# Performance work log

Measured on AMD Instinct MI355X. Metric: run time of the kernel, lower is better.

The kernel has to match this reference:

```python
import jax, jax.numpy as jnp
import numpy as np

# Problem geometry: B graphs of M atoms each (batch = repeat(arange(B), M)).
B, M, K = 1024, 256, 32          # graphs, atoms/graph, max_num_neighbors
CUTOFF_LOWER = 0.0
CUTOFF_UPPER = 5.0
BOX = 16.0                        # box side so ~30 neighbors within cutoff
BIG = 1e9                         # sentinel distance^2 for masked pairs


def setup_inputs() -> dict:
    key = jax.random.key(0)
    pos = jax.random.uniform(key, (B * M, 3), dtype=jnp.float32) * BOX
    batch = jnp.repeat(jnp.arange(B, dtype=jnp.int32), M)
    return {"pos": pos, "batch": batch}


def reference(pos, batch):
    # Fixed-size, jit-compatible radius_graph: per node keep the K nearest
    # neighbors within CUTOFF_UPPER (no self loops, loop=False). Invalid
    # (padded) edges get index -1, weight 0, vec 0.
    p = pos.reshape(B, M, 3)
    sq = jnp.sum(p * p, axis=-1)                                  # [B,M]
    d2 = sq[:, :, None] + sq[:, None, :] - 2.0 * jnp.einsum(
        'bmd,bnd->bmn', p, p)                                     # [B,M,M]
    d2 = jnp.maximum(d2, 0.0)
    self_mask = jnp.eye(M, dtype=bool)[None]
    invalid = self_mask | (d2 >= CUTOFF_UPPER ** 2)
    d2m = jnp.where(invalid, BIG, d2)
    neg_d2_sel, idx = jax.lax.top_k(-d2m, K)                      # [B,M,K]
    d2_sel = -neg_d2_sel
    valid = d2_sel < CUTOFF_UPPER ** 2
    w = jnp.sqrt(jnp.where(valid, d2_sel, 1.0))                   # safe sqrt
    valid = valid & (w >= CUTOFF_LOWER)                           # lower cutoff
    w = jnp.where(valid, w, 0.0)
    # edge_vec = pos[edge0] - pos[edge1] with edge0 = neighbor, edge1 = center
    nbr = jax.vmap(lambda pb, ib: pb[ib])(p, idx)                 # [B,M,K,3]
    vec = jnp.where(valid[..., None], nbr - p[:, :, None, :], 0.0)
    offs = (jnp.arange(B, dtype=jnp.int32) * M)[:, None, None]
    nbr_g = jnp.where(valid, idx.astype(jnp.int32) + offs, -1)
    ctr_g = jnp.where(
        valid, jnp.arange(M, dtype=jnp.int32)[None, :, None] + offs, -1)
    edge_index = jnp.stack([nbr_g.reshape(-1), ctr_g.reshape(-1)])  # [2, B*M*K]
    edge_weight = w.reshape(-1)                                     # [B*M*K]
    edge_vec = vec.reshape(-1, 3)                                   # [B*M*K,3]
    return edge_index, edge_weight, edge_vec
```

## Files before the change

### kernel.cpp

```cpp
#include <hip/hip_runtime.h>
#include <hip/hip_bf16.h>
#include <stdint.h>

#define NB 1024
#define NM 256
#define NK 32
#define CUT2 25.0f
#define CUTB 0x41C80000u
#define NCHUNK 4
#define CHUNK 64
#define CAP 28
#define TPB 128

__device__ __forceinline__ void bf16pk(float a, float b, float& ra, float& rb) {
  __hip_bfloat162 h = __float22bfloat162_rn(make_float2(a, b));
  uint32_t u;
  __builtin_memcpy(&u, &h, 4);
  ra = __uint_as_float(u << 16);
  rb = __uint_as_float(u & 0xFFFF0000u);
}

template <bool SELF>
__device__ __forceinline__ int scan_chunk(int ch, int cloc, const float4* sp,
                                          uint32_t* q32, int i, float xi,
                                          float yi, float zi, float sqi) {
  int cnt = 0;
#pragma unroll 8
  for (int t = 0; t < CHUNK; ++t) {
    const int j = ch * CHUNK + t;
    float4 pj = sp[j];
    float dot = __fmul_rn(xi, pj.x);
    dot = __builtin_fmaf(yi, pj.y, dot);
    dot = __builtin_fmaf(zi, pj.z, dot);
    float d2 = __fsub_rn(__fadd_rn(sqi, pj.w), __fmul_rn(2.0f, dot));
    d2 = fmaxf(d2, 0.0f);
    bool ok = (d2 < CUT2);
    if (SELF) ok = ok && (j != cloc);
    if (ok && cnt < CAP) {
      q32[cnt * TPB + i] = (__float_as_uint(d2) & 0xFFFFFF00u) | (uint32_t)j;
      ++cnt;
    }
  }
  return cnt;
}

__global__ __launch_bounds__(TPB, 4) void radius_graph_topk(
    const float* __restrict__ pos, float* __restrict__ out) {
  __shared__ __align__(16) unsigned char smem[4096 + CAP * TPB * 4];
  float4* sp = (float4*)smem;
  uint32_t* q32 = (uint32_t*)(smem + 4096);
  uint32_t* buf = q32;

  const int b = blockIdx.x;
  const int g = b >> 1;
  const int half = b & 1;
  const int i = threadIdx.x;
  const float* pg = pos + (size_t)g * NM * 3;

#pragma unroll
  for (int r = 0; r < 2; ++r) {
    const int a = r * TPB + i;
    const float x = pg[a * 3 + 0];
    const float y = pg[a * 3 + 1];
    const float z = pg[a * 3 + 2];
    const float sq = __fadd_rn(__fadd_rn(__fmul_rn(x, x), __fmul_rn(y, y)),
                               __fmul_rn(z, z));
    sp[a] = make_float4(x, y, z, sq);
  }
  __syncthreads();

  const int cloc = half * TPB + i;
  const float4 pcm = sp[cloc];
  const float xi = pcm.x, yi = pcm.y, zi = pcm.z, sqi = pcm.w;
  const int selfc = cloc >> 6;

  uint32_t key[NK];
#pragma unroll
  for (int s = 0; s < NK; ++s) key[s] = 0xFFFFFFFFu;

#pragma unroll
  for (int ch = 0; ch < NCHUNK; ++ch) {
    const int cnt =
        (ch == selfc)
            ? scan_chunk<true>(ch, cloc, sp, q32, i, xi, yi, zi, sqi)
            : scan_chunk<false>(ch, cloc, sp, q32, i, xi, yi, zi, sqi);
    uint32_t nxt = q32[i];
    for (int c = 0; c < cnt; ++c) {
      uint32_t cd = nxt;
      int cn = c + 1;
      cn = cn < CAP ? cn : 0;
      nxt = q32[cn * TPB + i];
#pragma unroll
      for (int s = 0; s < NK; ++s) {
        const uint32_t lo = cd < key[s] ? cd : key[s];
        cd = cd < key[s] ? key[s] : cd;
        key[s] = lo;
      }
    }
  }

  __syncthreads();

  const size_t BMK = (size_t)NB * NM * NK;
  float* o_nbr = out;
  float* o_ctr = out + BMK;
  float* o_w = out + 2 * BMK;
  float* o_v = out + 3 * BMK;
  const size_t E0 = ((size_t)g * NM + half * TPB) * NK;
  const int gbase = g * NM;

  for (int ph = 0; ph < 2; ++ph) {
    if ((i >> 6) == ph) {
      const int ci = i & 63;
      uint32_t* wb = buf + ci * 32;
#pragma unroll
      for (int sg = 0; sg < 8; ++sg) {
        *(uint4*)(wb + ((sg ^ (ci & 7)) << 2)) =
            make_uint4(key[sg * 4 + 0], key[sg * 4 + 1],
                       key[sg * 4 + 2], key[sg * 4 + 3]);
      }
    }
    __syncthreads();
#pragma unroll
    for (int it = 0; it < 4; ++it) {
      const int q = it * 512 + i * 4;
      const int cl = it * 16 + (i >> 3);
      const int gidx = i & 7;
      const uint4 kk4 =
          *(const uint4*)(buf + cl * 32 + ((gidx ^ (cl & 7)) << 2));
      const int cg_loc = half * TPB + ph * 64 + cl;
      const float4 pcc = sp[cg_loc];
      const float fctr = (float)(gbase + cg_loc);
      const uint32_t kks[4] = {kk4.x, kk4.y, kk4.z, kk4.w};
      float fn[4], fc[4], fw[4], vx[4], vy[4], vz[4];
#pragma unroll
      for (int u = 0; u < 4; ++u) {
        const uint32_t kk = kks[u];
        const bool v = kk < CUTB;
        const int j = (int)(kk & 0xFFu);
        const float d2m = __uint_as_float(kk & 0xFFFFFF00u);
        const float4 pj = sp[j];
        fn[u] = v ? (float)(gbase + j) : -1.0f;
        fc[u] = v ? fctr : -1.0f;
        fw[u] = v ? sqrtf(d2m) : 0.0f;
        vx[u] = v ? __fsub_rn(pj.x, pcc.x) : 0.0f;
        vy[u] = v ? __fsub_rn(pj.y, pcc.y) : 0.0f;
        vz[u] = v ? __fsub_rn(pj.z, pcc.z) : 0.0f;
      }
      float rn[4], rc[4], rw[4], rx[4], ry[4], rz[4];
#pragma unroll
      for (int u = 0; u < 4; u += 2) {
        bf16pk(fn[u], fn[u + 1], rn[u], rn[u + 1]);
        bf16pk(fc[u], fc[u + 1], rc[u], rc[u + 1]);
        bf16pk(fw[u], fw[u + 1], rw[u], rw[u + 1]);
        bf16pk(vx[u], vx[u + 1], rx[u], rx[u + 1]);
        bf16pk(vy[u], vy[u + 1], ry[u], ry[u + 1]);
        bf16pk(vz[u], vz[u + 1], rz[u], rz[u + 1]);
      }
      const size_t e = E0 + (size_t)ph * 2048 + (size_t)q;
      *(float4*)(o_nbr + e) = make_float4(rn[0], rn[1], rn[2], rn[3]);
      *(float4*)(o_ctr + e) = make_float4(rc[0], rc[1], rc[2], rc[3]);
      *(float4*)(o_w + e) = make_float4(rw[0], rw[1], rw[2], rw[3]);
      float* vp = o_v + e * 3;
      *(float4*)(vp + 0) = make_float4(rx[0], ry[0], rz[0], rx[1]);
      *(float4*)(vp + 4) = make_float4(ry[1], rz[1], rx[2], ry[2]);
      *(float4*)(vp + 8) = make_float4(rz[2], rx[3], ry[3], rz[3]);
    }
    __syncthreads();
  }
}

extern "C" void kernel_launch(void* const* d_in, const int* in_sizes, int n_in,
                              void* d_out, int out_size, void* d_ws,
                              size_t ws_size, hipStream_t stream) {
  const float* pos = (const float*)d_in[0];
  float* out = (float*)d_out;
  radius_graph_topk<<<NB * 2, TPB, 0, stream>>>(pos, out);
}
```

Baseline: 77.57 us.

## Use single-wave blocks processing two center quarters sequentially with wave barriers

Blocks shrink to one 64-thread wavefront. Each block still handles half a graph, but now does it as two sequential quarters of 64 centers, each running selection, key staging and output. The key staging buffer is separate from the candidate queue, and block-wide __syncthreads after the position load give way to wave barriers. This removes cross-wave barrier stalls and lets the selection of the next quarter overlap with other blocks' stores, at the cost of serializing two selections per thread and cutting per-block parallelism.

```diff
diff --git a/kernel.cpp b/kernel.cpp
--- a/kernel.cpp
+++ b/kernel.cpp
@@ -10,7 +10,7 @@
 #define NCHUNK 4
 #define CHUNK 64
 #define CAP 28
-#define TPB 128
+#define TPB 64
 
 __device__ __forceinline__ void bf16pk(float a, float b, float& ra, float& rb) {
   __hip_bfloat162 h = __float22bfloat162_rn(make_float2(a, b));
@@ -44,40 +44,13 @@
   return cnt;
 }
 
-__global__ __launch_bounds__(TPB, 4) void radius_graph_topk(
-    const float* __restrict__ pos, float* __restrict__ out) {
-  __shared__ __align__(16) unsigned char smem[4096 + CAP * TPB * 4];
-  float4* sp = (float4*)smem;
-  uint32_t* q32 = (uint32_t*)(smem + 4096);
-  uint32_t* buf = q32;
-
-  const int b = blockIdx.x;
-  const int g = b >> 1;
-  const int half = b & 1;
-  const int i = threadIdx.x;
-  const float* pg = pos + (size_t)g * NM * 3;
-
-#pragma unroll
-  for (int r = 0; r < 2; ++r) {
-    const int a = r * TPB + i;
-    const float x = pg[a * 3 + 0];
-    const float y = pg[a * 3 + 1];
-    const float z = pg[a * 3 + 2];
-    const float sq = __fadd_rn(__fadd_rn(__fmul_rn(x, x), __fmul_rn(y, y)),
-                               __fmul_rn(z, z));
-    sp[a] = make_float4(x, y, z, sq);
-  }
-  __syncthreads();
-
-  const int cloc = half * TPB + i;
+__device__ __forceinline__ void select_center(int cloc, int i, const float4* sp,
+                                              uint32_t* q32, uint32_t* key) {
   const float4 pcm = sp[cloc];
   const float xi = pcm.x, yi = pcm.y, zi = pcm.z, sqi = pcm.w;
   const int selfc = cloc >> 6;
-
-  uint32_t key[NK];
 #pragma unroll
   for (int s = 0; s < NK; ++s) key[s] = 0xFFFFFFFFu;
-
 #pragma unroll
   for (int ch = 0; ch < NCHUNK; ++ch) {
     const int cnt =
@@ -98,76 +71,113 @@
       }
     }
   }
+}
 
-  __syncthreads();
+__device__ __forceinline__ void stage_keys(int i, const uint32_t* key,
+                                           uint32_t* buf) {
+  uint32_t* wb = buf + i * 32;
+#pragma unroll
+  for (int sg = 0; sg < 8; ++sg) {
+    *(uint4*)(wb + ((sg ^ (i & 7)) << 2)) =
+        make_uint4(key[sg * 4 + 0], key[sg * 4 + 1], key[sg * 4 + 2],
+                   key[sg * 4 + 3]);
+  }
+}
 
+__device__ __forceinline__ void out_quarter(int g, int qbase, int i,
+                                            const float4* sp,
+                                            const uint32_t* buf,
+                                            float* __restrict__ out) {
   const size_t BMK = (size_t)NB * NM * NK;
   float* o_nbr = out;
   float* o_ctr = out + BMK;
   float* o_w = out + 2 * BMK;
   float* o_v = out + 3 * BMK;
-  const size_t E0 = ((size_t)g * NM + half * TPB) * NK;
   const int gbase = g * NM;
+#pragma unroll
+  for (int it = 0; it < 8; ++it) {
+    const int el = it * 256 + i * 4;
+    const int cl = it * 8 + (i >> 3);
+    const int gidx = i & 7;
+    const uint4 kk4 =
+        *(const uint4*)(buf + cl * 32 + ((gidx ^ (cl & 7)) << 2));
+    const int cg = qbase + cl;
+    const float4 pcc = sp[cg];
+    const float fctr = (float)(gbase + cg);
+    const uint32_t kks[4] = {kk4.x, kk4.y, kk4.z, kk4.w};
+    float fn[4], fc[4], fw[4], vx[4], vy[4], vz[4];
+#pragma unroll
+    for (int u = 0; u < 4; ++u) {
+      const uint32_t kk = kks[u];
+      const bool v = kk < CUTB;
+      const int j = (int)(kk & 0xFFu);
+      const float d2m = __uint_as_float(kk & 0xFFFFFF00u);
+      const float4 pj = sp[j];
+      fn[u] = v ? (float)(gbase + j) : -1.0f;
+      fc[u] = v ? fctr : -1.0f;
+      fw[u] = v ? sqrtf(d2m) : 0.0f;
+      vx[u] = v ? __fsub_rn(pj.x, pcc.x) : 0.0f;
+      vy[u] = v ? __fsub_rn(pj.y, pcc.y) : 0.0f;
+      vz[u] = v ? __fsub_rn(pj.z, pcc.z) : 0.0f;
+    }
+    float rn[4], rc[4], rw[4], rx[4], ry[4], rz[4];
+#pragma unroll
+    for (int u = 0; u < 4; u += 2) {
+      bf16pk(fn[u], fn[u + 1], rn[u], rn[u + 1]);
+      bf16pk(fc[u], fc[u + 1], rc[u], rc[u + 1]);
+      bf16pk(fw[u], fw[u + 1], rw[u], rw[u + 1]);
+      bf16pk(vx[u], vx[u + 1], rx[u], rx[u + 1]);
+      bf16pk(vy[u], vy[u + 1], ry[u], ry[u + 1]);
+      bf16pk(vz[u], vz[u + 1], rz[u], rz[u + 1]);
+    }
+    const size_t e = (size_t)g * (NM * NK) + (size_t)qbase * NK + el;
+    *(float4*)(o_nbr + e) = make_float4(rn[0], rn[1], rn[2], rn[3]);
+    *(float4*)(o_ctr + e) = make_float4(rc[0], rc[1], rc[2], rc[3]);
+    *(float4*)(o_w + e) = make_float4(rw[0], rw[1], rw[2], rw[3]);
+    float* vp = o_v + e * 3;
+    *(float4*)(vp + 0) = make_float4(rx[0], ry[0], rz[0], rx[1]);
+    *(float4*)(vp + 4) = make_float4(ry[1], rz[1], rx[2], ry[2]);
+    *(float4*)(vp + 8) = make_float4(rz[2], rx[3], ry[3], rz[3]);
+  }
+}
 
-  for (int ph = 0; ph < 2; ++ph) {
-    if ((i >> 6) == ph) {
-      const int ci = i & 63;
-      uint32_t* wb = buf + ci * 32;
+__global__ __launch_bounds__(TPB, 2) void radius_graph_topk(
+    const float* __restrict__ pos, float* __restrict__ out) {
+  __shared__ __align__(16) unsigned char smem[19456];
+  float4* sp = (float4*)smem;
+  uint32_t* q32 = (uint32_t*)(smem + 4096);
+  uint32_t* buf = (uint32_t*)(smem + 11264);
+
+  const int g = blockIdx.x >> 1;
+  const int half = blockIdx.x & 1;
+  const int i = threadIdx.x;
+  const float* pg = pos + (size_t)g * NM * 3;
+
 #pragma unroll
-      for (int sg = 0; sg < 8; ++sg) {
-        *(uint4*)(wb + ((sg ^ (ci & 7)) << 2)) =
-            make_uint4(key[sg * 4 + 0], key[sg * 4 + 1],
-                       key[sg * 4 + 2], key[sg * 4 + 3]);
-      }
-    }
-    __syncthreads();
-#pragma unroll
-    for (int it = 0; it < 4; ++it) {
-      const int q = it * 512 + i * 4;
-      const int cl = it * 16 + (i >> 3);
-      const int gidx = i & 7;
-      const uint4 kk4 =
-          *(const uint4*)(buf + cl * 32 + ((gidx ^ (cl & 7)) << 2));
-      const int cg_loc = half * TPB + ph * 64 + cl;
-      const float4 pcc = sp[cg_loc];
-      const float fctr = (float)(gbase + cg_loc);
-      const uint32_t kks[4] = {kk4.x, kk4.y, kk4.z, kk4.w};
-      float fn[4], fc[4], fw[4], vx[4], vy[4], vz[4];
-#pragma unroll
-      for (int u = 0; u < 4; ++u) {
-        const uint32_t kk = kks[u];
-        const bool v = kk < CUTB;
-        const int j = (int)(kk & 0xFFu);
-        const float d2m = __uint_as_float(kk & 0xFFFFFF00u);
-        const float4 pj = sp[j];
-        fn[u] = v ? (float)(gbase + j) : -1.0f;
-        fc[u] = v ? fctr : -1.0f;
-        fw[u] = v ? sqrtf(d2m) : 0.0f;
-        vx[u] = v ? __fsub_rn(pj.x, pcc.x) : 0.0f;
-        vy[u] = v ? __fsub_rn(pj.y, pcc.y) : 0.0f;
-        vz[u] = v ? __fsub_rn(pj.z, pcc.z) : 0.0f;
-      }
-      float rn[4], rc[4], rw[4], rx[4], ry[4], rz[4];
-#pragma unroll
-      for (int u = 0; u < 4; u += 2) {
-        bf16pk(fn[u], fn[u + 1], rn[u], rn[u + 1]);
-        bf16pk(fc[u], fc[u + 1], rc[u], rc[u + 1]);
-        bf16pk(fw[u], fw[u + 1], rw[u], rw[u + 1]);
-        bf16pk(vx[u], vx[u + 1], rx[u], rx[u + 1]);
-        bf16pk(vy[u], vy[u + 1], ry[u], ry[u + 1]);
-        bf16pk(vz[u], vz[u + 1], rz[u], rz[u + 1]);
-      }
-      const size_t e = E0 + (size_t)ph * 2048 + (size_t)q;
-      *(float4*)(o_nbr + e) = make_float4(rn[0], rn[1], rn[2], rn[3]);
-      *(float4*)(o_ctr + e) = make_float4(rc[0], rc[1], rc[2], rc[3]);
-      *(float4*)(o_w + e) = make_float4(rw[0], rw[1], rw[2], rw[3]);
-      float* vp = o_v + e * 3;
-      *(float4*)(vp + 0) = make_float4(rx[0], ry[0], rz[0], rx[1]);
-      *(float4*)(vp + 4) = make_float4(ry[1], rz[1], rx[2], ry[2]);
-      *(float4*)(vp + 8) = make_float4(rz[2], rx[3], ry[3], rz[3]);
-    }
-    __syncthreads();
+  for (int r = 0; r < 4; ++r) {
+    const int a = r * TPB + i;
+    const float x = pg[a * 3 + 0];
+    const float y = pg[a * 3 + 1];
+    const float z = pg[a * 3 + 2];
+    const float sq = __fadd_rn(__fadd_rn(__fmul_rn(x, x), __fmul_rn(y, y)),
+                               __fmul_rn(z, z));
+    sp[a] = make_float4(x, y, z, sq);
   }
+  __syncthreads();
+
+  const int base = half * 128;
+  uint32_t key[NK];
+
+  select_center(base + i, i, sp, q32, key);
+  stage_keys(i, key, buf);
+  __builtin_amdgcn_wave_barrier();
+  out_quarter(g, base, i, sp, buf, out);
+
+  select_center(base + 64 + i, i, sp, q32, key);
+  __builtin_amdgcn_wave_barrier();
+  stage_keys(i, key, buf);
+  __builtin_amdgcn_wave_barrier();
+  out_quarter(g, base + 64, i, sp, buf, out);
 }
 
 extern "C" void kernel_launch(void* const* d_in, const int* in_sizes, int n_in,
```

After: 97.12 us. +25.2%, slower.
